# Performance work log

Measured on AMD Instinct MI355X. Metric: run time of the kernel, lower is better.

Reference implementation:

```python
import jax, jax.numpy as jnp
import numpy as np

TEMPERATURE = 0.15
SINKHORN_ITERS = 5
CHUNKS = 8
DIM = 4096
CHUNK_SIZE = DIM // CHUNKS


def _sinkhorn(logits, num_iters=SINKHORN_ITERS):
    # Alternating row (dim=-1) then column (dim=-2) log-normalization, matching torch order.
    log_p = logits
    for _ in range(num_iters):
        log_p = log_p - jax.nn.logsumexp(log_p, axis=-1, keepdims=True)
        log_p = log_p - jax.nn.logsumexp(log_p, axis=-2, keepdims=True)
    return jnp.exp(log_p)


def setup_inputs() -> dict:
    key = jax.random.key(0)
    k1, k2, k3 = jax.random.split(key, 3)
    x = jax.random.normal(k1, (4, 4096, DIM), dtype=jnp.float32)
    chunk_logits = 0.01 * jax.random.normal(k2, (CHUNKS, CHUNKS), dtype=jnp.float32)
    intra_logits = 0.01 * jax.random.normal(k3, (CHUNKS, CHUNK_SIZE, CHUNK_SIZE), dtype=jnp.float32)
    return {"x": x, "chunk_logits": chunk_logits, "intra_logits": intra_logits}


def reference(x, chunk_logits, intra_logits):
    orig_shape = x.shape
    y = x.reshape(-1, CHUNKS, CHUNK_SIZE)  # [B, c, d]
    chunk_perm = _sinkhorn(chunk_logits / TEMPERATURE)  # [c, c]
    y = jnp.einsum('ij,bjd->bid', chunk_perm, y)
    intra_perm = _sinkhorn(intra_logits / TEMPERATURE)  # [c, d, d]
    # out[b,c,k] = sum_j y[b,c,j] * intra_perm[c,k,j]  (y @ intra_perm^T per chunk)
    y = jnp.einsum('bcj,ckj->bck', y, intra_perm)
    return y.reshape(orig_shape)
```

## Files before the change

kernel.cpp:

```cpp
#include <hip/hip_runtime.h>
#include <cstdint>
#include <cstddef>

typedef unsigned short u16;
typedef __bf16 bf16x8 __attribute__((ext_vector_type(8)));
typedef float f32x4 __attribute__((ext_vector_type(4)));
typedef u16 u16x8 __attribute__((ext_vector_type(8)));

typedef const void __attribute__((address_space(1)))* gas_ptr;
typedef void __attribute__((address_space(3)))* las_ptr;

#define TEMP_INV (1.0f / 0.15f)
#define NCH 8
#define CS 512
#define DIM 4096
#define NSLAB 16

__device__ __forceinline__ u16 f2bf(float f) {
  union { float f; uint32_t u; } a; a.f = f;
  uint32_t r = a.u + 0x7fffu + ((a.u >> 16) & 1u);
  return (u16)(r >> 16);
}

__global__ __launch_bounds__(256) void re_kernel(
    const float* __restrict__ chunk_logits,
    const float* __restrict__ intra_logits,
    float* __restrict__ cp,
    float* __restrict__ E,
    float* __restrict__ u)
{
  const int bid = blockIdx.x;
  const int tid = threadIdx.x;

  if (bid == NCH * 128) {
    if (tid < 64) {
      float e = __expf(chunk_logits[tid] * TEMP_INV);
      float v = 1.0f, uu = 0.0f;
      #pragma unroll
      for (int it = 0; it < 5; ++it) {
        float t = e * v;
        t += __shfl_xor(t, 1); t += __shfl_xor(t, 2); t += __shfl_xor(t, 4);
        uu = 1.0f / t;
        float t2 = e * uu;
        t2 += __shfl_xor(t2, 8); t2 += __shfl_xor(t2, 16); t2 += __shfl_xor(t2, 32);
        v = 1.0f / t2;
      }
      cp[tid] = e * uu * v;
    }
    return;
  }

  const int c = bid >> 7;
  const int w = tid >> 6, l = tid & 63;
  const int row = ((bid & 127) << 2) + w;
  const float* Lr = intra_logits + ((size_t)c * CS + row) * CS;
  float* Er = E + ((size_t)c * CS + row) * CS;

  float s = 0.0f;
  #pragma unroll
  for (int rd = 0; rd < 2; ++rd) {
    const int j = rd * 256 + l * 4;
    float4 t = *(const float4*)(Lr + j);
    float4 e;
    e.x = __expf(t.x * TEMP_INV); e.y = __expf(t.y * TEMP_INV);
    e.z = __expf(t.z * TEMP_INV); e.w = __expf(t.w * TEMP_INV);
    *(float4*)(Er + j) = e;
    s += e.x + e.y + e.z + e.w;
  }
  s += __shfl_xor(s, 1);  s += __shfl_xor(s, 2);  s += __shfl_xor(s, 4);
  s += __shfl_xor(s, 8);  s += __shfl_xor(s, 16); s += __shfl_xor(s, 32);
  if (l == 0) u[c * CS + row] = 1.0f / s;
}

__global__ __launch_bounds__(256) void c1_kernel(
    const float* __restrict__ E,
    const float* __restrict__ u,
    float* __restrict__ partial)
{
  const int bid = blockIdx.x;
  const int c  = bid >> 5;
  const int ks = (bid >> 1) & 15;
  const int jt = bid & 1;
  const int j  = jt * 256 + threadIdx.x;
  const float* Ec = E + (size_t)c * CS * CS;

  __shared__ float us[32];
  if (threadIdx.x < 32) us[threadIdx.x] = u[c * CS + ks * 32 + threadIdx.x];
  __syncthreads();

  float s = 0.0f;
  #pragma unroll 8
  for (int kk = 0; kk < 32; ++kk)
    s += Ec[(size_t)(ks * 32 + kk) * CS + j] * us[kk];
  partial[((size_t)c * NSLAB + ks) * CS + j] = s;
}

__global__ __launch_bounds__(256) void r_kernel(
    const float* __restrict__ E,
    const float* __restrict__ partial,
    float* __restrict__ u)
{
  const int bid = blockIdx.x;
  const int tid = threadIdx.x;
  const int c = bid >> 7;
  const float* pc = partial + (size_t)c * NSLAB * CS;

  __shared__ float vs[CS];
  #pragma unroll
  for (int rep = 0; rep < 2; ++rep) {
    const int j = rep * 256 + tid;
    float s = 0.0f;
    #pragma unroll
    for (int sl = 0; sl < NSLAB; ++sl) s += pc[sl * CS + j];
    vs[j] = 1.0f / s;
  }
  __syncthreads();

  const int w = tid >> 6, l = tid & 63;
  const int row = ((bid & 127) << 2) + w;
  const float* Er = E + ((size_t)c * CS + row) * CS;
  float s = 0.0f;
  #pragma unroll
  for (int rd = 0; rd < 2; ++rd) {
    const int j = rd * 256 + l * 4;
    float4 e = *(const float4*)(Er + j);
    float4 v = *(const float4*)(vs + j);
    s += e.x * v.x + e.y * v.y + e.z * v.z + e.w * v.w;
  }
  s += __shfl_xor(s, 1);  s += __shfl_xor(s, 2);  s += __shfl_xor(s, 4);
  s += __shfl_xor(s, 8);  s += __shfl_xor(s, 16); s += __shfl_xor(s, 32);
  if (l == 0) u[c * CS + row] = 1.0f / s;
}

__global__ __launch_bounds__(256) void p_kernel(
    const float* __restrict__ E,
    const float* __restrict__ partial,
    const float* __restrict__ u,
    u16* __restrict__ P)
{
  const int bid = blockIdx.x;
  const int tid = threadIdx.x;
  const int c = bid >> 7;
  const float* pc = partial + (size_t)c * NSLAB * CS;

  __shared__ float vs[CS];
  #pragma unroll
  for (int rep = 0; rep < 2; ++rep) {
    const int j = rep * 256 + tid;
    float s = 0.0f;
    #pragma unroll
    for (int sl = 0; sl < NSLAB; ++sl) s += pc[sl * CS + j];
    vs[j] = 1.0f / s;
  }
  __syncthreads();

  const int w = tid >> 6, l = tid & 63;
  const int row = ((bid & 127) << 2) + w;
  const float uu = u[c * CS + row];
  const float* Er = E + ((size_t)c * CS + row) * CS;
  u16* Pr = P + ((size_t)c * CS + row) * CS;

  const int j0 = l * 8;
  float4 e0 = *(const float4*)(Er + j0);
  float4 e1 = *(const float4*)(Er + j0 + 4);
  float4 v0 = *(const float4*)(vs + j0);
  float4 v1 = *(const float4*)(vs + j0 + 4);
  u16x8 o;
  o[0] = f2bf(e0.x * uu * v0.x); o[1] = f2bf(e0.y * uu * v0.y);
  o[2] = f2bf(e0.z * uu * v0.z); o[3] = f2bf(e0.w * uu * v0.w);
  o[4] = f2bf(e1.x * uu * v1.x); o[5] = f2bf(e1.y * uu * v1.y);
  o[6] = f2bf(e1.z * uu * v1.z); o[7] = f2bf(e1.w * uu * v1.w);
  *(u16x8*)(Pr + j0) = o;
}

__global__ __launch_bounds__(256) void stage1_kernel(
    const float* __restrict__ x,
    const float* __restrict__ cp,
    u16* __restrict__ y)
{
  __shared__ float cps[64];
  const int tid = threadIdx.x;
  if (tid < 64) cps[tid] = cp[tid];
  __syncthreads();

  const int g  = blockIdx.x * 256 + tid;
  const int b  = g >> 7;
  const int d4 = g & 127;

  const float4* xr = (const float4*)x + (size_t)b * 1024 + d4;
  float4 xi[8];
  #pragma unroll
  for (int jc = 0; jc < 8; ++jc) xi[jc] = xr[(size_t)jc * 128];

  ushort4* yr = (ushort4*)y + (size_t)b * 1024 + d4;
  #pragma unroll
  for (int i = 0; i < 8; ++i) {
    float ax = 0.f, ay = 0.f, az = 0.f, aw = 0.f;
    #pragma unroll
    for (int jc = 0; jc < 8; ++jc) {
      const float wgt = cps[i * 8 + jc];
      ax += wgt * xi[jc].x; ay += wgt * xi[jc].y;
      az += wgt * xi[jc].z; aw += wgt * xi[jc].w;
    }
    ushort4 o;
    o.x = f2bf(ax); o.y = f2bf(ay); o.z = f2bf(az); o.w = f2bf(aw);
    yr[(size_t)i * 128] = o;
  }
}

#define BM 128
#define BN 128
#define BK 32

__global__ __launch_bounds__(256) void gemm_kernel(
    const u16* __restrict__ Y,
    const u16* __restrict__ P,
    float* __restrict__ out)
{
  __shared__ u16 As[BM * BK];
  __shared__ u16 Bs[BN * BK];

  const int tid = threadIdx.x;
  const int m0 = blockIdx.x * BM;
  const int n0 = blockIdx.y * BN;
  const int c  = blockIdx.z;

  const u16* Ab = Y + (size_t)m0 * DIM + (size_t)c * CS;
  const u16* Bb = P + (size_t)c * CS * CS + (size_t)n0 * CS;

  const int w = tid >> 6, l = tid & 63;
  const int wm = (w >> 1) * 64, wn = (w & 1) * 64;
  const int lrow = l & 15, lk = (l >> 4) * 8;
  const int colb = (tid & 3) * 8;

  f32x4 acc[4][4] = {};

  for (int k0 = 0; k0 < CS; k0 += BK) {
    #pragma unroll
    for (int rd = 0; rd < 2; ++rd) {
      const int idx = rd * 256 + tid;
      const int r = idx >> 2;
      const u16* g = Ab + (size_t)r * DIM + k0 + colb;
      u16* lds = As + ((idx >> 6) << 6) * 8;
      __builtin_amdgcn_global_load_lds((gas_ptr)g, (las_ptr)lds, 16, 0, 0);
    }
    #pragma unroll
    for (int rd = 0; rd < 2; ++rd) {
      const int idx = rd * 256 + tid;
      const int r = idx >> 2;
      const u16* g = Bb + (size_t)r * CS + k0 + colb;
      u16* lds = Bs + ((idx >> 6) << 6) * 8;
      __builtin_amdgcn_global_load_lds((gas_ptr)g, (las_ptr)lds, 16, 0, 0);
    }
    __syncthreads();

    bf16x8 af[4], bfr[4];
    #pragma unroll
    for (int mi = 0; mi < 4; ++mi)
      af[mi] = *(const bf16x8*)&As[(wm + mi * 16 + lrow) * BK + lk];
    #pragma unroll
    for (int ni = 0; ni < 4; ++ni)
      bfr[ni] = *(const bf16x8*)&Bs[(wn + ni * 16 + lrow) * BK + lk];

    #pragma unroll
    for (int mi = 0; mi < 4; ++mi)
      #pragma unroll
      for (int ni = 0; ni < 4; ++ni)
        acc[mi][ni] = __builtin_amdgcn_mfma_f32_16x16x32_bf16(
            af[mi], bfr[ni], acc[mi][ni], 0, 0, 0);
    __syncthreads();
  }

  const int ccol = l & 15, rquad = (l >> 4) * 4;
  #pragma unroll
  for (int mi = 0; mi < 4; ++mi) {
    #pragma unroll
    for (int ni = 0; ni < 4; ++ni) {
      #pragma unroll
      for (int r = 0; r < 4; ++r) {
        const int mm = m0 + wm + mi * 16 + rquad + r;
        const int nn = n0 + wn + ni * 16 + ccol;
        out[(size_t)mm * DIM + (size_t)c * CS + nn] = acc[mi][ni][r];
      }
    }
  }
}

extern "C" void kernel_launch(void* const* d_in, const int* in_sizes, int n_in,
                              void* d_out, int out_size, void* d_ws, size_t ws_size,
                              hipStream_t stream) {
  const float* x  = (const float*)d_in[0];
  const float* cl = (const float*)d_in[1];
  const float* il = (const float*)d_in[2];
  float* out = (float*)d_out;

  char* ws = (char*)d_ws;
  float* cp      = (float*)ws;
  float* u       = (float*)(ws + 1024);
  float* partial = (float*)(ws + 32 * 1024);
  u16*   P       = (u16*)(ws + 512 * 1024);
  float* E       = (float*)(ws + (size_t)8 * 1024 * 1024);
  u16*   Y       = (u16*)(ws + (size_t)8 * 1024 * 1024);

  const int rows = in_sizes[0] / DIM;

  re_kernel<<<dim3(NCH * 128 + 1), dim3(256), 0, stream>>>(cl, il, cp, E, u);
  for (int it = 0; it < 4; ++it) {
    c1_kernel<<<dim3(256), dim3(256), 0, stream>>>(E, u, partial);
    r_kernel<<<dim3(1024), dim3(256), 0, stream>>>(E, partial, u);
  }
  c1_kernel<<<dim3(256), dim3(256), 0, stream>>>(E, u, partial);
  p_kernel<<<dim3(1024), dim3(256), 0, stream>>>(E, partial, u, P);

  stage1_kernel<<<dim3(rows / 2), dim3(256), 0, stream>>>(x, cp, Y);
  gemm_kernel<<<dim3(rows / BM, CS / BN, NCH), dim3(256), 0, stream>>>(Y, P, out);
}
```

Baseline: 636.5 us.

## Fuse Sinkhorn and chunk-mix into one prep kernel; double-buffer and swizzle GEMM

Replaces the chain of twelve small Sinkhorn launches and the separate chunk-mixing kernel with one prep kernel. Eight blocks each run a whole chunk's Sinkhorn iterations in shared memory, recomputing exp from the logits instead of storing E. The remaining blocks do the chunk mix into bf16 Y. The GEMM gains double-buffered LDS with XOR-swizzled columns, swapped MFMA operands so each lane holds four contiguous outputs, and vectorised nontemporal stores. The risk is that the Sinkhorn work now runs on only eight blocks serially, recomputing exp many times, which may become the critical path while the other blocks handle the mixing.

```diff
diff --git a/kernel.cpp b/kernel.cpp
--- a/kernel.cpp
+++ b/kernel.cpp
@@ -14,7 +14,6 @@
 #define NCH 8
 #define CS 512
 #define DIM 4096
-#define NSLAB 16
 
 __device__ __forceinline__ u16 f2bf(float f) {
   union { float f; uint32_t u; } a; a.f = f;
@@ -22,168 +21,130 @@
   return (u16)(r >> 16);
 }
 
-__global__ __launch_bounds__(256) void re_kernel(
+__device__ __forceinline__ float wave_sum(float s) {
+  s += __shfl_xor(s, 1);  s += __shfl_xor(s, 2);  s += __shfl_xor(s, 4);
+  s += __shfl_xor(s, 8);  s += __shfl_xor(s, 16); s += __shfl_xor(s, 32);
+  return s;
+}
+
+__global__ __launch_bounds__(1024) void prep_kernel(
+    const float* __restrict__ x,
     const float* __restrict__ chunk_logits,
     const float* __restrict__ intra_logits,
-    float* __restrict__ cp,
-    float* __restrict__ E,
-    float* __restrict__ u)
+    u16* __restrict__ P,
+    u16* __restrict__ Y)
 {
+  __shared__ float u_s[CS];
+  __shared__ float v_s[CS];
+  __shared__ float ps[8][CS];
+  __shared__ float cps[64];
+
   const int bid = blockIdx.x;
   const int tid = threadIdx.x;
 
-  if (bid == NCH * 128) {
-    if (tid < 64) {
-      float e = __expf(chunk_logits[tid] * TEMP_INV);
-      float v = 1.0f, uu = 0.0f;
+  if (bid < NCH) {
+    const int c = bid;
+    const int wv = tid >> 6, l = tid & 63;
+    const float* Lc = intra_logits + (size_t)c * CS * CS;
+
+    for (int r = wv; r < CS; r += 16) {
+      const float* Lr = Lc + (size_t)r * CS;
+      float s = 0.0f;
       #pragma unroll
-      for (int it = 0; it < 5; ++it) {
-        float t = e * v;
-        t += __shfl_xor(t, 1); t += __shfl_xor(t, 2); t += __shfl_xor(t, 4);
-        uu = 1.0f / t;
-        float t2 = e * uu;
-        t2 += __shfl_xor(t2, 8); t2 += __shfl_xor(t2, 16); t2 += __shfl_xor(t2, 32);
-        v = 1.0f / t2;
-      }
-      cp[tid] = e * uu * v;
+      for (int rd = 0; rd < 2; ++rd) {
+        const int j = rd * 256 + l * 4;
+        float4 t = *(const float4*)(Lr + j);
+        s += __expf(t.x * TEMP_INV) + __expf(t.y * TEMP_INV)
+           + __expf(t.z * TEMP_INV) + __expf(t.w * TEMP_INV);
+      }
+      s = wave_sum(s);
+      if (l == 0) u_s[r] = 1.0f / s;
+    }
+    __syncthreads();
+
+    for (int it = 0; it < 5; ++it) {
+      {
+        const int cq = (tid & 127) * 4, slab = tid >> 7;
+        const float* Ls = Lc + (size_t)slab * 64 * CS + cq;
+        float ax = 0.f, ay = 0.f, az = 0.f, aw = 0.f;
+        #pragma unroll 8
+        for (int rr = 0; rr < 64; ++rr) {
+          float4 t = *(const float4*)(Ls + (size_t)rr * CS);
+          const float uu = u_s[slab * 64 + rr];
+          ax += __expf(t.x * TEMP_INV) * uu;
+          ay += __expf(t.y * TEMP_INV) * uu;
+          az += __expf(t.z * TEMP_INV) * uu;
+          aw += __expf(t.w * TEMP_INV) * uu;
+        }
+        float4 a; a.x = ax; a.y = ay; a.z = az; a.w = aw;
+        *(float4*)&ps[slab][cq] = a;
+      }
+      __syncthreads();
+      if (tid < CS) {
+        float s = 0.0f;
+        #pragma unroll
+        for (int sl = 0; sl < 8; ++sl) s += ps[sl][tid];
+        v_s[tid] = 1.0f / s;
+      }
+      __syncthreads();
+      if (it == 4) break;
+      for (int r = wv; r < CS; r += 16) {
+        const float* Lr = Lc + (size_t)r * CS;
+        float s = 0.0f;
+        #pragma unroll
+        for (int rd = 0; rd < 2; ++rd) {
+          const int j = rd * 256 + l * 4;
+          float4 t = *(const float4*)(Lr + j);
+          float4 v = *(const float4*)(v_s + j);
+          s += __expf(t.x * TEMP_INV) * v.x + __expf(t.y * TEMP_INV) * v.y
+             + __expf(t.z * TEMP_INV) * v.z + __expf(t.w * TEMP_INV) * v.w;
+        }
+        s = wave_sum(s);
+        if (l == 0) u_s[r] = 1.0f / s;
+      }
+      __syncthreads();
+    }
+
+    for (int r = wv; r < CS; r += 16) {
+      const float uu = u_s[r];
+      const float* Lr = Lc + (size_t)r * CS;
+      u16* Pr = P + ((size_t)c * CS + r) * CS;
+      const int j0 = l * 8;
+      float4 t0 = *(const float4*)(Lr + j0);
+      float4 t1 = *(const float4*)(Lr + j0 + 4);
+      float4 v0 = *(const float4*)(v_s + j0);
+      float4 v1 = *(const float4*)(v_s + j0 + 4);
+      u16x8 o;
+      o[0] = f2bf(__expf(t0.x * TEMP_INV) * uu * v0.x);
+      o[1] = f2bf(__expf(t0.y * TEMP_INV) * uu * v0.y);
+      o[2] = f2bf(__expf(t0.z * TEMP_INV) * uu * v0.z);
+      o[3] = f2bf(__expf(t0.w * TEMP_INV) * uu * v0.w);
+      o[4] = f2bf(__expf(t1.x * TEMP_INV) * uu * v1.x);
+      o[5] = f2bf(__expf(t1.y * TEMP_INV) * uu * v1.y);
+      o[6] = f2bf(__expf(t1.z * TEMP_INV) * uu * v1.z);
+      o[7] = f2bf(__expf(t1.w * TEMP_INV) * uu * v1.w);
+      *(u16x8*)(Pr + j0) = o;
     }
     return;
   }
 
-  const int c = bid >> 7;
-  const int w = tid >> 6, l = tid & 63;
-  const int row = ((bid & 127) << 2) + w;
-  const float* Lr = intra_logits + ((size_t)c * CS + row) * CS;
-  float* Er = E + ((size_t)c * CS + row) * CS;
-
-  float s = 0.0f;
-  #pragma unroll
-  for (int rd = 0; rd < 2; ++rd) {
-    const int j = rd * 256 + l * 4;
-    float4 t = *(const float4*)(Lr + j);
-    float4 e;
-    e.x = __expf(t.x * TEMP_INV); e.y = __expf(t.y * TEMP_INV);
-    e.z = __expf(t.z * TEMP_INV); e.w = __expf(t.w * TEMP_INV);
-    *(float4*)(Er + j) = e;
-    s += e.x + e.y + e.z + e.w;
-  }
-  s += __shfl_xor(s, 1);  s += __shfl_xor(s, 2);  s += __shfl_xor(s, 4);
-  s += __shfl_xor(s, 8);  s += __shfl_xor(s, 16); s += __shfl_xor(s, 32);
-  if (l == 0) u[c * CS + row] = 1.0f / s;
-}
-
-__global__ __launch_bounds__(256) void c1_kernel(
-    const float* __restrict__ E,
-    const float* __restrict__ u,
-    float* __restrict__ partial)
-{
-  const int bid = blockIdx.x;
-  const int c  = bid >> 5;
-  const int ks = (bid >> 1) & 15;
-  const int jt = bid & 1;
-  const int j  = jt * 256 + threadIdx.x;
-  const float* Ec = E + (size_t)c * CS * CS;
-
-  __shared__ float us[32];
-  if (threadIdx.x < 32) us[threadIdx.x] = u[c * CS + ks * 32 + threadIdx.x];
+  if (tid < 64) {
+    float e = __expf(chunk_logits[tid] * TEMP_INV);
+    float v = 1.0f, uu = 0.0f;
+    #pragma unroll
+    for (int it = 0; it < 5; ++it) {
+      float t = e * v;
+      t += __shfl_xor(t, 1); t += __shfl_xor(t, 2); t += __shfl_xor(t, 4);
+      uu = 1.0f / t;
+      float t2 = e * uu;
+      t2 += __shfl_xor(t2, 8); t2 += __shfl_xor(t2, 16); t2 += __shfl_xor(t2, 32);
+      v = 1.0f / t2;
+    }
+    cps[tid] = e * uu * v;
+  }
   __syncthreads();
 
-  float s = 0.0f;
-  #pragma unroll 8
-  for (int kk = 0; kk < 32; ++kk)
-    s += Ec[(size_t)(ks * 32 + kk) * CS + j] * us[kk];
-  partial[((size_t)c * NSLAB + ks) * CS + j] = s;
-}
-
-__global__ __launch_bounds__(256) void r_kernel(
-    const float* __restrict__ E,
-    const float* __restrict__ partial,
-    float* __restrict__ u)
-{
-  const int bid = blockIdx.x;
-  const int tid = threadIdx.x;
-  const int c = bid >> 7;
-  const float* pc = partial + (size_t)c * NSLAB * CS;
-
-  __shared__ float vs[CS];
-  #pragma unroll
-  for (int rep = 0; rep < 2; ++rep) {
-    const int j = rep * 256 + tid;
-    float s = 0.0f;
-    #pragma unroll
-    for (int sl = 0; sl < NSLAB; ++sl) s += pc[sl * CS + j];
-    vs[j] = 1.0f / s;
-  }
-  __syncthreads();
-
-  const int w = tid >> 6, l = tid & 63;
-  const int row = ((bid & 127) << 2) + w;
-  const float* Er = E + ((size_t)c * CS + row) * CS;
-  float s = 0.0f;
-  #pragma unroll
-  for (int rd = 0; rd < 2; ++rd) {
-    const int j = rd * 256 + l * 4;
-    float4 e = *(const float4*)(Er + j);
-    float4 v = *(const float4*)(vs + j);
-    s += e.x * v.x + e.y * v.y + e.z * v.z + e.w * v.w;
-  }
-  s += __shfl_xor(s, 1);  s += __shfl_xor(s, 2);  s += __shfl_xor(s, 4);
-  s += __shfl_xor(s, 8);  s += __shfl_xor(s, 16); s += __shfl_xor(s, 32);
-  if (l == 0) u[c * CS + row] = 1.0f / s;
-}
-
-__global__ __launch_bounds__(256) void p_kernel(
-    const float* __restrict__ E,
-    const float* __restrict__ partial,
-    const float* __restrict__ u,
-    u16* __restrict__ P)
-{
-  const int bid = blockIdx.x;
-  const int tid = threadIdx.x;
-  const int c = bid >> 7;
-  const float* pc = partial + (size_t)c * NSLAB * CS;
-
-  __shared__ float vs[CS];
-  #pragma unroll
-  for (int rep = 0; rep < 2; ++rep) {
-    const int j = rep * 256 + tid;
-    float s = 0.0f;
-    #pragma unroll
-    for (int sl = 0; sl < NSLAB; ++sl) s += pc[sl * CS + j];
-    vs[j] = 1.0f / s;
-  }
-  __syncthreads();
-
-  const int w = tid >> 6, l = tid & 63;
-  const int row = ((bid & 127) << 2) + w;
-  const float uu = u[c * CS + row];
-  const float* Er = E + ((size_t)c * CS + row) * CS;
-  u16* Pr = P + ((size_t)c * CS + row) * CS;
-
-  const int j0 = l * 8;
-  float4 e0 = *(const float4*)(Er + j0);
-  float4 e1 = *(const float4*)(Er + j0 + 4);
-  float4 v0 = *(const float4*)(vs + j0);
-  float4 v1 = *(const float4*)(vs + j0 + 4);
-  u16x8 o;
-  o[0] = f2bf(e0.x * uu * v0.x); o[1] = f2bf(e0.y * uu * v0.y);
-  o[2] = f2bf(e0.z * uu * v0.z); o[3] = f2bf(e0.w * uu * v0.w);
-  o[4] = f2bf(e1.x * uu * v1.x); o[5] = f2bf(e1.y * uu * v1.y);
-  o[6] = f2bf(e1.z * uu * v1.z); o[7] = f2bf(e1.w * uu * v1.w);
-  *(u16x8*)(Pr + j0) = o;
-}
-
-__global__ __launch_bounds__(256) void stage1_kernel(
-    const float* __restrict__ x,
-    const float* __restrict__ cp,
-    u16* __restrict__ y)
-{
-  __shared__ float cps[64];
-  const int tid = threadIdx.x;
-  if (tid < 64) cps[tid] = cp[tid];
-  __syncthreads();
-
-  const int g  = blockIdx.x * 256 + tid;
+  const int g  = (bid - NCH) * 1024 + tid;
   const int b  = g >> 7;
   const int d4 = g & 127;
 
@@ -192,7 +153,7 @@
   #pragma unroll
   for (int jc = 0; jc < 8; ++jc) xi[jc] = xr[(size_t)jc * 128];
 
-  ushort4* yr = (ushort4*)y + (size_t)b * 1024 + d4;
+  ushort4* yr = (ushort4*)Y + (size_t)b * 1024 + d4;
   #pragma unroll
   for (int i = 0; i < 8; ++i) {
     float ax = 0.f, ay = 0.f, az = 0.f, aw = 0.f;
@@ -211,14 +172,15 @@
 #define BM 128
 #define BN 128
 #define BK 32
+#define NT (CS / BK)
 
 __global__ __launch_bounds__(256) void gemm_kernel(
     const u16* __restrict__ Y,
     const u16* __restrict__ P,
     float* __restrict__ out)
 {
-  __shared__ u16 As[BM * BK];
-  __shared__ u16 Bs[BN * BK];
+  __shared__ u16 As[2][BM * BK];
+  __shared__ u16 Bs[2][BN * BK];
 
   const int tid = threadIdx.x;
   const int m0 = blockIdx.x * BM;
@@ -226,62 +188,71 @@
   const int c  = blockIdx.z;
 
   const u16* Ab = Y + (size_t)m0 * DIM + (size_t)c * CS;
-  const u16* Bb = P + (size_t)c * CS * CS + (size_t)n0 * CS;
+  const u16* Bb = P + ((size_t)c * CS + n0) * CS;
 
   const int w = tid >> 6, l = tid & 63;
   const int wm = (w >> 1) * 64, wn = (w & 1) * 64;
-  const int lrow = l & 15, lk = (l >> 4) * 8;
-  const int colb = (tid & 3) * 8;
+  const int lrow = l & 15, sub = l >> 4;
 
   f32x4 acc[4][4] = {};
 
-  for (int k0 = 0; k0 < CS; k0 += BK) {
+  auto stage = [&](int buf, int kk) {
     #pragma unroll
     for (int rd = 0; rd < 2; ++rd) {
       const int idx = rd * 256 + tid;
       const int r = idx >> 2;
-      const u16* g = Ab + (size_t)r * DIM + k0 + colb;
-      u16* lds = As + ((idx >> 6) << 6) * 8;
-      __builtin_amdgcn_global_load_lds((gas_ptr)g, (las_ptr)lds, 16, 0, 0);
+      const int cb = ((idx & 3) ^ (r & 3)) << 3;
+      __builtin_amdgcn_global_load_lds((gas_ptr)(Ab + (size_t)r * DIM + kk + cb),
+                                       (las_ptr)(&As[buf][(idx & ~63) * 8]), 16, 0, 0);
     }
     #pragma unroll
     for (int rd = 0; rd < 2; ++rd) {
       const int idx = rd * 256 + tid;
       const int r = idx >> 2;
-      const u16* g = Bb + (size_t)r * CS + k0 + colb;
-      u16* lds = Bs + ((idx >> 6) << 6) * 8;
-      __builtin_amdgcn_global_load_lds((gas_ptr)g, (las_ptr)lds, 16, 0, 0);
-    }
-    __syncthreads();
-
-    bf16x8 af[4], bfr[4];
-    #pragma unroll
-    for (int mi = 0; mi < 4; ++mi)
-      af[mi] = *(const bf16x8*)&As[(wm + mi * 16 + lrow) * BK + lk];
-    #pragma unroll
-    for (int ni = 0; ni < 4; ++ni)
-      bfr[ni] = *(const bf16x8*)&Bs[(wn + ni * 16 + lrow) * BK + lk];
+      const int cb = ((idx & 3) ^ (r & 3)) << 3;
+      __builtin_amdgcn_global_load_lds((gas_ptr)(Bb + (size_t)r * CS + kk + cb),
+                                       (las_ptr)(&Bs[buf][(idx & ~63) * 8]), 16, 0, 0);
+    }
+  };
+
+  stage(0, 0);
+  __syncthreads();
+
+  int cur = 0;
+  for (int t = 0; t < NT; ++t) {
+    if (t + 1 < NT) stage(cur ^ 1, (t + 1) * BK);
+
+    bf16x8 yf[4], pf[4];
+    #pragma unroll
+    for (int mi = 0; mi < 4; ++mi) {
+      const int row = wm + mi * 16 + lrow;
+      yf[mi] = *(const bf16x8*)&As[cur][row * BK + ((sub ^ (row & 3)) << 3)];
+    }
+    #pragma unroll
+    for (int ni = 0; ni < 4; ++ni) {
+      const int row = wn + ni * 16 + lrow;
+      pf[ni] = *(const bf16x8*)&Bs[cur][row * BK + ((sub ^ (row & 3)) << 3)];
+    }
 
     #pragma unroll
     for (int mi = 0; mi < 4; ++mi)
       #pragma unroll
       for (int ni = 0; ni < 4; ++ni)
         acc[mi][ni] = __builtin_amdgcn_mfma_f32_16x16x32_bf16(
-            af[mi], bfr[ni], acc[mi][ni], 0, 0, 0);
+            pf[ni], yf[mi], acc[mi][ni], 0, 0, 0);
+
     __syncthreads();
-  }
-
-  const int ccol = l & 15, rquad = (l >> 4) * 4;
+    cur ^= 1;
+  }
+
+  const int nq = sub * 4;
   #pragma unroll
   for (int mi = 0; mi < 4; ++mi) {
+    const size_t mrow = (size_t)(m0 + wm + mi * 16 + lrow) * DIM + (size_t)c * CS;
     #pragma unroll
     for (int ni = 0; ni < 4; ++ni) {
-      #pragma unroll
-      for (int r = 0; r < 4; ++r) {
-        const int mm = m0 + wm + mi * 16 + rquad + r;
-        const int nn = n0 + wn + ni * 16 + ccol;
-        out[(size_t)mm * DIM + (size_t)c * CS + nn] = acc[mi][ni][r];
-      }
+      __builtin_nontemporal_store(acc[mi][ni],
+          (f32x4*)(out + mrow + (size_t)(n0 + wn + ni * 16 + nq)));
     }
   }
 }
@@ -295,23 +266,11 @@
   float* out = (float*)d_out;
 
   char* ws = (char*)d_ws;
-  float* cp      = (float*)ws;
-  float* u       = (float*)(ws + 1024);
-  float* partial = (float*)(ws + 32 * 1024);
-  u16*   P       = (u16*)(ws + 512 * 1024);
-  float* E       = (float*)(ws + (size_t)8 * 1024 * 1024);
-  u16*   Y       = (u16*)(ws + (size_t)8 * 1024 * 1024);
+  u16* P = (u16*)ws;
+  u16* Y = (u16*)(ws + (size_t)8 * 1024 * 1024);
 
   const int rows = in_sizes[0] / DIM;
 
-  re_kernel<<<dim3(NCH * 128 + 1), dim3(256), 0, stream>>>(cl, il, cp, E, u);
-  for (int it = 0; it < 4; ++it) {
-    c1_kernel<<<dim3(256), dim3(256), 0, stream>>>(E, u, partial);
-    r_kernel<<<dim3(1024), dim3(256), 0, stream>>>(E, partial, u);
-  }
-  c1_kernel<<<dim3(256), dim3(256), 0, stream>>>(E, u, partial);
-  p_kernel<<<dim3(1024), dim3(256), 0, stream>>>(E, partial, u, P);
-
-  stage1_kernel<<<dim3(rows / 2), dim3(256), 0, stream>>>(x, cp, Y);
+  prep_kernel<<<dim3(NCH + rows / 8), dim3(1024), 0, stream>>>(x, cl, il, P, Y);
   gemm_kernel<<<dim3(rows / BM, CS / BN, NCH), dim3(256), 0, stream>>>(Y, P, out);
 }
```

New measurement: 687.8 us. 8.1% more time.
